# Kernel optimization log

Measured on AMD Instinct MI355X. Metric: run time of the kernel, lower is better.

The kernel has to match this reference:

```python
import jax, jax.numpy as jnp
import numpy as np

B, C, H, W = 8, 256, 64, 64
NH = 4
HD = C // NH
EPS_LN = 1e-5
EPS_NORM = 1e-12


def ln2d(x, w, b):
    # LayerNorm over channel dim of NCHW, per spatial location
    m = jnp.mean(x, axis=1, keepdims=True)
    v = jnp.mean((x - m) ** 2, axis=1, keepdims=True)
    return (x - m) / jnp.sqrt(v + EPS_LN) * w[None, :, None, None] + b[None, :, None, None]


def l2norm(x):
    # F.normalize(x, dim=-1)
    n = jnp.sqrt(jnp.sum(x * x, axis=-1, keepdims=True))
    return x / jnp.maximum(n, EPS_NORM)


def setup_inputs() -> dict:
    key = jax.random.key(0)
    ks = jax.random.split(key, 12)
    s = 0.02
    return {
        "img_feat": jax.random.normal(ks[0], (B, C, H, W), jnp.float32),
        "aux0": jax.random.normal(ks[1], (B, C, H, W), jnp.float32),
        "aux1": jax.random.normal(ks[2], (B, C, H, W), jnp.float32),
        "q_ln_w": jnp.ones((C,), jnp.float32),
        "q_ln_b": jnp.zeros((C,), jnp.float32),
        "kv_ln_w": jnp.ones((C,), jnp.float32),
        "kv_ln_b": jnp.zeros((C,), jnp.float32),
        "Wq": jax.random.normal(ks[3], (C, C), jnp.float32) * s,
        "Wkv": jax.random.normal(ks[4], (2 * C, C), jnp.float32) * s,
        "Wo": jax.random.normal(ks[5], (C, C), jnp.float32) * s,
        "bo": jnp.zeros((C,), jnp.float32),
        "attn_scale": jnp.zeros((NH, 1, 1), jnp.float32),
        "mlp_ln_w": jnp.ones((C,), jnp.float32),
        "mlp_ln_b": jnp.zeros((C,), jnp.float32),
        "W1": jax.random.normal(ks[6], (C, C), jnp.float32) * s,
        "b1": jnp.zeros((C,), jnp.float32),
        "W2": jax.random.normal(ks[7], (C, C), jnp.float32) * s,
        "b2": jnp.zeros((C,), jnp.float32),
    }


def reference(img_feat, aux0, aux1, q_ln_w, q_ln_b, kv_ln_w, kv_ln_b,
              Wq, Wkv, Wo, bo, attn_scale, mlp_ln_w, mlp_ln_b, W1, b1, W2, b2):
    HWn = H * W
    # q branch
    q = ln2d(img_feat, q_ln_w, q_ln_b).reshape(B, C, HWn)
    q = jnp.einsum('oc,bcn->bon', Wq, q).reshape(B, NH, HD, HWn)
    # kv branch: cat aux feats along batch (2B)
    kv_in = jnp.concatenate([aux0, aux1], axis=0)
    kv = ln2d(kv_in, kv_ln_w, kv_ln_b).reshape(2 * B, C, HWn)
    kv = jnp.einsum('oc,bcn->bon', Wkv, kv).reshape(2 * B, 2, NH, HD, HWn)
    k, v = kv[:, 0], kv[:, 1]  # each (2B, nh, hd, hw)
    qn = l2norm(q)
    kn = l2norm(k)
    kt, kd = kn[:B], kn[B:]
    vt, vd = v[:B], v[B:]
    # transposed (cross-covariance) cosine attention: hd x hd score matrix
    tex_attn = jax.nn.softmax(jnp.einsum('bnch,bndh->bncd', qn, kt), axis=-1)
    dep_attn = jax.nn.softmax(jnp.einsum('bnch,bndh->bncd', qn, kd), axis=-1)
    tex_qkv = jnp.einsum('bncd,bndh->bnch', tex_attn, vt)
    dep_qkv = jnp.einsum('bncd,bndh->bnch', dep_attn, vd)
    gate = jax.nn.sigmoid(attn_scale)[None]  # (1, nh, 1, 1)
    qkv = gate * tex_qkv + (1.0 - gate) * dep_qkv  # (B, nh, hd, hw)
    qkv = qkv.reshape(B, C, HWn)
    o = jnp.einsum('oc,bcn->bon', Wo, qkv).reshape(B, C, H, W) + bo[None, :, None, None]
    x = img_feat + o
    # ConvMlp (norm_ffn): LayerNorm2d -> 1x1 conv -> GELU -> 1x1 conv
    y = ln2d(x, mlp_ln_w, mlp_ln_b).reshape(B, C, HWn)
    y = jnp.einsum('oc,bcn->bon', W1, y) + b1[None, :, None]
    y = jax.nn.gelu(y)
    y = jnp.einsum('oc,bcn->bon', W2, y) + b2[None, :, None]
    return x + y.reshape(B, C, H, W)
```

## Files before the change

kernel.cpp:

```cpp
#include <hip/hip_runtime.h>
#include <math.h>
#include <stdint.h>

#define B_   8
#define C_   256
#define N_   4096

typedef __bf16 bf16;
typedef __bf16 bf16x8 __attribute__((ext_vector_type(8)));
typedef __bf16 bf16x4 __attribute__((ext_vector_type(4)));
typedef float  f32x4  __attribute__((ext_vector_type(4)));

#define MFMA16(a, b, c) __builtin_amdgcn_mfma_f32_16x16x32_bf16((a), (b), (c), 0, 0, 0)

struct Ptrs { const void* p[18]; };

__device__ __forceinline__ f32x4 ld4(const void* p, long i, bool f32) {
    f32x4 r;
    if (f32) {
        r = *(const f32x4*)((const float*)p + i);
    } else {
        bf16x4 v = *(const bf16x4*)((const bf16*)p + i);
        r[0] = (float)v[0]; r[1] = (float)v[1]; r[2] = (float)v[2]; r[3] = (float)v[3];
    }
    return r;
}

__device__ __forceinline__ float wave_sum(float s) {
    #pragma unroll
    for (int off = 32; off; off >>= 1) s += __shfl_xor(s, off);
    return s;
}

__device__ __forceinline__ void gl_lds16(const bf16* g, bf16* l) {
    __builtin_amdgcn_global_load_lds(
        (const __attribute__((address_space(1))) void*)(uintptr_t)g,
        (__attribute__((address_space(3))) void*)(uintptr_t)l, 16, 0, 0);
}

__global__ __launch_bounds__(256) void prep_kernel(Ptrs a, bf16* __restrict__ wb,
                                                   float* __restrict__ Sbuf,
                                                   bf16* __restrict__ biasb) {
    bool f32 = ((const unsigned*)a.p[3])[0] == 0x3F800000u;
    int row = blockIdx.x * 4 + (threadIdx.x >> 6);
    int lane = threadIdx.x & 63;
    long c4 = lane * 4;
    if (row >= 1536) {
        if (row == 1539) {
            if (lane == 0) {
                f32x4 v = ld4(a.p[11], 0, f32);
                #pragma unroll
                for (int j = 0; j < 4; ++j) biasb[768 + j] = (bf16)v[j];
            }
        } else {
            const void* s = (row == 1536) ? a.p[10] : (row == 1537) ? a.p[15] : a.p[17];
            f32x4 v = ld4(s, c4, f32);
            bf16x4 o;
            #pragma unroll
            for (int j = 0; j < 4; ++j) o[j] = (bf16)v[j];
            *(bf16x4*)(biasb + (row - 1536) * 256 + c4) = o;
        }
        return;
    }
    const void *W, *lw = nullptr, *lb = nullptr;
    long wrow; bf16* dst; float *s1 = nullptr, *s2 = nullptr;
    if (row < 256)       { W = a.p[7];  lw = a.p[3];  lb = a.p[4];  wrow = row;        dst = wb + row * 256;                 s1 = Sbuf + row;          s2 = Sbuf + 256 + row; }
    else if (row < 768)  { W = a.p[8];  lw = a.p[5];  lb = a.p[6];  wrow = row - 256;  dst = wb + 65536 + wrow * 256;        s1 = Sbuf + 512 + wrow;   s2 = Sbuf + 1024 + wrow; }
    else if (row < 1024) { W = a.p[14]; lw = a.p[12]; lb = a.p[13]; wrow = row - 768;  dst = wb + 196608 + wrow * 256;       s1 = Sbuf + 1536 + wrow;  s2 = Sbuf + 1792 + wrow; }
    else if (row < 1280) { W = a.p[9];  wrow = row - 1024; dst = wb + 262144 + wrow * 256; }
    else                 { W = a.p[16]; wrow = row - 1280; dst = wb + 327680 + wrow * 256; }
    f32x4 W4 = ld4(W, wrow * 256 + c4, f32);
    f32x4 w4, b4;
    if (lw) { w4 = ld4(lw, c4, f32); b4 = ld4(lb, c4, f32); }
    else    { w4[0]=w4[1]=w4[2]=w4[3]=1.f; b4[0]=b4[1]=b4[2]=b4[3]=0.f; }
    bf16x4 o;
    float s1v = 0.f, s2v = 0.f;
    #pragma unroll
    for (int j = 0; j < 4; ++j) {
        float wp = W4[j] * w4[j];
        o[j] = (bf16)wp;
        s1v += wp;
        s2v += W4[j] * b4[j];
    }
    *(bf16x4*)(dst + c4) = o;
    if (s1) {
        s1v = wave_sum(s1v); s2v = wave_sum(s2v);
        if (lane == 0) { *s1 = s1v; *s2 = s2v; }
    }
}

__global__ __launch_bounds__(256) void transpose_kernel(Ptrs a, bf16* __restrict__ xT,
                                                        float2* __restrict__ st) {
    bool f32 = ((const unsigned*)a.p[3])[0] == 0x3F800000u;
    int gt = blockIdx.z;
    const void* src; int batch;
    if (gt < 8)       { src = a.p[0]; batch = gt; }
    else if (gt < 16) { src = a.p[1]; batch = gt - 8; }
    else              { src = a.p[2]; batch = gt - 16; }
    int n0 = blockIdx.x * 64;
    int t = threadIdx.x;
    __shared__ float T[64][68];
    int cl = t >> 4, n4 = (t & 15) * 4;
    int chunk = t & 7, nr = t >> 3;
    float sa[2] = {0.f, 0.f}, qa[2] = {0.f, 0.f};
    for (int ct = 0; ct < 4; ++ct) {
        int c0 = ct * 64;
        if (ct) __syncthreads();
        #pragma unroll
        for (int i = 0; i < 4; ++i) {
            int c = i * 16 + cl;
            f32x4 v = ld4(src, ((long)batch * 256 + c0 + c) * 4096 + n0 + n4, f32);
            #pragma unroll
            for (int j = 0; j < 4; ++j) {
                int nn = n4 + j;
                T[nn][c ^ (((nn >> 2) & 3) << 3)] = v[j];
            }
        }
        __syncthreads();
        #pragma unroll
        for (int j = 0; j < 2; ++j) {
            int n = j * 32 + nr;
            int cs = (chunk * 8) ^ (((n >> 2) & 3) << 3);
            const f32x4* p = (const f32x4*)&T[n][cs];
            f32x4 lo = p[0], hi = p[1];
            bf16x8 o;
            #pragma unroll
            for (int jj = 0; jj < 4; ++jj) { o[jj] = (bf16)lo[jj]; o[4 + jj] = (bf16)hi[jj]; }
            *(bf16x8*)(xT + ((size_t)gt * 4096 + n0 + n) * 256 + c0 + chunk * 8) = o;
            #pragma unroll
            for (int jj = 0; jj < 8; ++jj) { float f = (float)o[jj]; sa[j] += f; qa[j] += f * f; }
        }
    }
    #pragma unroll
    for (int j = 0; j < 2; ++j) {
        float s = sa[j], q = qa[j];
        #pragma unroll
        for (int off = 1; off < 8; off <<= 1) { s += __shfl_xor(s, off); q += __shfl_xor(q, off); }
        if (chunk == 0) {
            float mean = s * (1.0f / 256.0f);
            float var  = q * (1.0f / 256.0f) - mean * mean;
            float2 o2; o2.x = mean; o2.y = rsqrtf(var + 1e-5f);
            st[(size_t)gt * 4096 + n0 + j * 32 + nr] = o2;
        }
    }
}

__global__ __launch_bounds__(256) void statsT_kernel(const bf16* __restrict__ xT,
                                                     float2* __restrict__ st) {
    int row = blockIdx.x * 4 + (threadIdx.x >> 6);
    int lane = threadIdx.x & 63;
    bf16x4 v = *(const bf16x4*)(xT + (size_t)row * 256 + lane * 4);
    float s = 0.f, q = 0.f;
    #pragma unroll
    for (int j = 0; j < 4; ++j) { float f = (float)v[j]; s += f; q += f * f; }
    s = wave_sum(s); q = wave_sum(q);
    if (lane == 0) {
        float mean = s * (1.0f / 256.0f);
        float var  = q * (1.0f / 256.0f) - mean * mean;
        float2 o; o.x = mean; o.y = rsqrtf(var + 1e-5f);
        st[row] = o;
    }
}

__global__ __launch_bounds__(256, 2) void wgemm_kernel(const bf16* __restrict__ A,
                                                    const bf16* __restrict__ xT,
                                                    const float2* __restrict__ stats,
                                                    const float* __restrict__ S1,
                                                    const float* __restrict__ S2,
                                                    const bf16* __restrict__ bias,
                                                    const bf16* __restrict__ resT,
                                                    void* __restrict__ out,
                                                    bf16* __restrict__ vT,
                                                    const unsigned* __restrict__ probe,
                                                    int emode, int gelu) {
    int n0 = blockIdx.x * 128;
    int ot = blockIdx.y;
    int g  = blockIdx.z;
    int t = threadIdx.x, wv = t >> 6, lane = t & 63;
    int m16 = lane & 15, quad = lane >> 4;
    int wr = wv >> 1, wc = wv & 1;
    int rl = lane >> 3, slot = lane & 7;

    __shared__ bf16 As[2][128 * 64];
    __shared__ bf16 Bs[2][128 * 64];

    const bf16* Agbase = A + (size_t)ot * 128 * 256;
    const bf16* Bgbase = xT + ((size_t)g * 4096 + n0) * 256;

    auto stage = [&](int buf, int ks) {
        #pragma unroll
        for (int i = 0; i < 4; ++i) {
            int row = wv * 32 + i * 8 + rl;
            int koff = ks * 64 + ((slot ^ (row & 7)) << 3);
            gl_lds16(Agbase + (size_t)row * 256 + koff, &As[buf][(wv * 32 + i * 8) * 64]);
            gl_lds16(Bgbase + (size_t)row * 256 + koff, &Bs[buf][(wv * 32 + i * 8) * 64]);
        }
    };

    f32x4 acc[4][4];
    #pragma unroll
    for (int i = 0; i < 4; ++i)
        #pragma unroll
        for (int j = 0; j < 4; ++j) acc[i][j] = (f32x4){0.f, 0.f, 0.f, 0.f};

    auto compute = [&](int buf) {
        #pragma unroll
        for (int kf = 0; kf < 2; ++kf) {
            bf16x8 af[4], bv[4];
            #pragma unroll
            for (int mt = 0; mt < 4; ++mt) {
                int r = wr * 64 + mt * 16 + m16;
                af[mt] = *(const bf16x8*)&As[buf][r * 64 + (((kf * 4 + quad) ^ (r & 7)) << 3)];
            }
            #pragma unroll
            for (int nt = 0; nt < 4; ++nt) {
                int r = wc * 64 + nt * 16 + m16;
                bv[nt] = *(const bf16x8*)&Bs[buf][r * 64 + (((kf * 4 + quad) ^ (r & 7)) << 3)];
            }
            #pragma unroll
            for (int mt = 0; mt < 4; ++mt)
                #pragma unroll
                for (int nt = 0; nt < 4; ++nt)
                    acc[mt][nt] = MFMA16(af[mt], bv[nt], acc[mt][nt]);
        }
    };

    stage(0, 0);
    stage(1, 1);
    #pragma unroll
    for (int ks = 0; ks < 4; ++ks) {
        if (ks < 3) asm volatile("s_waitcnt vmcnt(8)" ::: "memory");
        else        asm volatile("s_waitcnt vmcnt(0)" ::: "memory");
        __builtin_amdgcn_sched_barrier(0);
        __builtin_amdgcn_s_barrier();
        compute(ks & 1);
        __builtin_amdgcn_s_barrier();
        if (ks < 2) stage(ks & 1, ks + 2);
    }

    int of32 = (emode == 3) ? (probe[0] == 0x3F800000u) : 0;

    #pragma unroll
    for (int mt = 0; mt < 4; ++mt) {
        int olb  = wr * 64 + mt * 16 + quad * 4;
        int orow = ot * 128 + olb;
        f32x4 s1v, s2v, bz;
        if (stats) { s1v = *(const f32x4*)(S1 + orow); s2v = *(const f32x4*)(S2 + orow); }
        if (bias) {
            bf16x4 bb = *(const bf16x4*)(bias + orow);
            #pragma unroll
            for (int r = 0; r < 4; ++r) bz[r] = (float)bb[r];
        }
        #pragma unroll
        for (int nt = 0; nt < 4; ++nt) {
            int n = n0 + wc * 64 + nt * 16 + m16;
            f32x4 v = acc[mt][nt];
            if (stats) {
                float2 st = stats[(size_t)g * N_ + n];
                float a1 = st.y, a2 = -st.y * st.x;
                #pragma unroll
                for (int r = 0; r < 4; ++r) v[r] = a1 * v[r] + a2 * s1v[r] + s2v[r];
            }
            if (bias) {
                #pragma unroll
                for (int r = 0; r < 4; ++r) v[r] += bz[r];
            }
            if (gelu) {
                #pragma unroll
                for (int r = 0; r < 4; ++r) {
                    float x = v[r];
                    float u = x + 0.044715f * x * x * x;
                    v[r] = 0.5f * x * (1.0f + tanhf(0.7978845608028654f * u));
                }
            }
            if (emode == 0) {
                if (vT == nullptr || orow < 256) {
                    bf16* o = (bf16*)out;
                    #pragma unroll
                    for (int r = 0; r < 4; ++r)
                        o[((size_t)(g * 256 + orow + r)) * N_ + n] = (bf16)v[r];
                } else {
                    int od = orow - 256;
                    int hh = od >> 6, d0 = od & 63;
                    bf16x4 tmp;
                    #pragma unroll
                    for (int r = 0; r < 4; ++r) tmp[r] = (bf16)v[r];
                    *(bf16x4*)(vT + (((size_t)(g * 4 + hh)) * N_ + n) * 64 + d0) = tmp;
                }
            } else if (emode == 2) {
                size_t idx = ((size_t)g * N_ + n) * 256 + orow;
                if (resT) {
                    bf16x4 rr = *(const bf16x4*)(resT + idx);
                    #pragma unroll
                    for (int r = 0; r < 4; ++r) v[r] += (float)rr[r];
                }
                bf16x4 tmp;
                #pragma unroll
                for (int r = 0; r < 4; ++r) tmp[r] = (bf16)v[r];
                *(bf16x4*)((bf16*)out + idx) = tmp;
            } else {
                bf16x4 rr = *(const bf16x4*)(resT + ((size_t)g * N_ + n) * 256 + orow);
                #pragma unroll
                for (int r = 0; r < 4; ++r) {
                    float val = v[r] + (float)rr[r];
                    size_t oi = ((size_t)(g * 256 + orow + r)) * N_ + n;
                    if (of32) ((float*)out)[oi] = val;
                    else      ((bf16*)out)[oi] = (bf16)val;
                }
            }
        }
    }
}

__global__ __launch_bounds__(256) void rownorm_kernel(const bf16* __restrict__ x,
                                                      float* __restrict__ invn) {
    size_t row = blockIdx.x;
    const bf16* p = x + (row << 12);
    int t = threadIdx.x;
    float s = 0.f;
    #pragma unroll
    for (int i = 0; i < 2; ++i) {
        bf16x8 v = *(const bf16x8*)(p + ((size_t)(i * 256 + t) << 3));
        #pragma unroll
        for (int j = 0; j < 8; ++j) { float f = (float)v[j]; s += f * f; }
    }
    #pragma unroll
    for (int off = 32; off > 0; off >>= 1) s += __shfl_down(s, off);
    __shared__ float ps[4];
    if ((t & 63) == 0) ps[t >> 6] = s;
    __syncthreads();
    if (t == 0) {
        float tot = ps[0] + ps[1] + ps[2] + ps[3];
        invn[row] = 1.0f / fmaxf(sqrtf(tot), 1e-12f);
    }
}

__global__ __launch_bounds__(256) void sgemm_kernel(const bf16* __restrict__ q,
                                                    const bf16* __restrict__ k,
                                                    float* __restrict__ Spart) {
    int bh = blockIdx.x, ks = blockIdx.y;
    int b = bh >> 2, h = bh & 3;
    int t = threadIdx.x, wv = t >> 6, lane = t & 63;
    int m16 = lane & 15, quad = lane >> 4;
    const bf16* qrow = q + (size_t)(b * 256 + h * 64 + wv * 16 + m16) * N_;
    const bf16* kt0  = k + (size_t)(b * 256 + h * 64) * N_;
    const bf16* kd0  = k + (size_t)((b + 8) * 256 + h * 64) * N_;

    f32x4 at[4], ad[4];
    #pragma unroll
    for (int i = 0; i < 4; ++i) { at[i] = (f32x4){0.f,0.f,0.f,0.f}; ad[i] = (f32x4){0.f,0.f,0.f,0.f}; }

    int nbeg = ks * 512;
    for (int n = nbeg; n < nbeg + 512; n += 32) {
        int ko = n + quad * 8;
        bf16x8 a = *(const bf16x8*)(qrow + ko);
        #pragma unroll
        for (int dt = 0; dt < 4; ++dt) {
            bf16x8 bt = *(const bf16x8*)(kt0 + (size_t)(dt * 16 + m16) * N_ + ko);
            at[dt] = MFMA16(a, bt, at[dt]);
            bf16x8 bd = *(const bf16x8*)(kd0 + (size_t)(dt * 16 + m16) * N_ + ko);
            ad[dt] = MFMA16(a, bd, ad[dt]);
        }
    }
    float* oT = Spart + (size_t)(ks * 32 + bh) * 4096;
    float* oD = Spart + (size_t)8 * 32 * 4096 + (size_t)(ks * 32 + bh) * 4096;
    #pragma unroll
    for (int dt = 0; dt < 4; ++dt)
        #pragma unroll
        for (int r = 0; r < 4; ++r) {
            int c = wv * 16 + quad * 4 + r, d = dt * 16 + m16;
            oT[c * 64 + d] = at[dt][r];
            oD[c * 64 + d] = ad[dt][r];
        }
}

__global__ __launch_bounds__(256) void softmax_kernel(const float* __restrict__ Spart,
                                                      const float* __restrict__ invnq,
                                                      const float* __restrict__ invnk,
                                                      const bf16* __restrict__ attn_scale,
                                                      bf16* __restrict__ Acat) {
    int bh = blockIdx.x;
    int h = bh & 3;
    int t = threadIdx.x, wv = t >> 6, lane = t & 63;
    float g = 1.0f / (1.0f + expf(-(float)attn_scale[h]));
    #pragma unroll
    for (int i = 0; i < 4; ++i) {
        int idx = blockIdx.y * 16 + wv * 4 + i;
        int stream = idx >> 6, c = idx & 63;
        const float* Sp = Spart + (size_t)stream * 8 * 32 * 4096 + (size_t)bh * 4096 + c * 64 + lane;
        float s = 0.f;
        #pragma unroll
        for (int ks = 0; ks < 8; ++ks) s += Sp[(size_t)ks * 32 * 4096];
        s *= invnq[bh * 64 + c] * invnk[(stream ? bh + 32 : bh) * 64 + lane];
        float mx = s;
        #pragma unroll
        for (int off = 32; off > 0; off >>= 1) mx = fmaxf(mx, __shfl_xor(mx, off));
        float e = expf(s - mx);
        float sum = e;
        #pragma unroll
        for (int off = 32; off > 0; off >>= 1) sum += __shfl_xor(sum, off);
        float a = e / sum * (stream == 0 ? g : 1.0f - g);
        Acat[(size_t)bh * 8192 + c * 128 + stream * 64 + lane] = (bf16)a;
    }
}

__global__ __launch_bounds__(256) void av_kernel(const bf16* __restrict__ Acat,
                                                 const bf16* __restrict__ vT,
                                                 bf16* __restrict__ qkvT) {
    int pt = blockIdx.x, h = blockIdx.y, b = blockIdx.z;
    int bh = b * 4 + h;
    int t = threadIdx.x, wv = t >> 6, lane = t & 63;
    int m16 = lane & 15, quad = lane >> 4;
    int p0 = pt * 64;

    const bf16* Arow = Acat + (size_t)bh * 8192 + (size_t)(wv * 16 + m16) * 128 + quad * 8;
    bf16x8 a[4];
    #pragma unroll
    for (int ds = 0; ds < 4; ++ds) a[ds] = *(const bf16x8*)(Arow + ds * 32);

    f32x4 acc[4];
    #pragma unroll
    for (int i = 0; i < 4; ++i) acc[i] = (f32x4){0.f,0.f,0.f,0.f};

    #pragma unroll
    for (int nt = 0; nt < 4; ++nt) {
        int p = p0 + nt * 16 + m16;
        #pragma unroll
        for (int ds = 0; ds < 4; ++ds) {
            int stream = ds >> 1;
            int dl = (ds & 1) * 32 + quad * 8;
            const bf16* vb = vT + (((size_t)(b + 8 * stream) * 4 + h) * N_ + p) * 64 + dl;
            bf16x8 bv = *(const bf16x8*)vb;
            acc[nt] = MFMA16(a[ds], bv, acc[nt]);
        }
    }
    #pragma unroll
    for (int nt = 0; nt < 4; ++nt) {
        int p = p0 + nt * 16 + m16;
        int cbase = h * 64 + wv * 16 + quad * 4;
        bf16x4 o;
        #pragma unroll
        for (int r = 0; r < 4; ++r) o[r] = (bf16)acc[nt][r];
        *(bf16x4*)(qkvT + ((size_t)b * 4096 + p) * 256 + cbase) = o;
    }
}

extern "C" void kernel_launch(void* const* d_in, const int* in_sizes, int n_in,
                              void* d_out, int out_size, void* d_ws, size_t ws_size,
                              hipStream_t stream) {
    (void)in_sizes; (void)n_in; (void)out_size; (void)ws_size;

    Ptrs args;
    for (int i = 0; i < 18; ++i) args.p[i] = d_in[i];
    const unsigned* probe = (const unsigned*)d_in[3];

    char* ws = (char*)d_ws;
    size_t off = 0;
    auto alloc = [&](size_t bytes) { char* p = ws + off; off += (bytes + 255) & ~(size_t)255; return p; };
    bf16*   xTall = (bf16*)alloc(50331648);
    float2* stAll = (float2*)alloc(786432);
    float2* stX   = (float2*)alloc(262144);
    bf16*   wb    = (bf16*)alloc(786432);
    float*  Sbuf  = (float*)alloc(8192);
    bf16*   biasb = (bf16*)alloc(2048);
    bf16*   q     = (bf16*)alloc(16777216);
    bf16*   k     = (bf16*)alloc(33554432);
    bf16*   vT    = (bf16*)alloc(33554432);
    float*  Spart = (float*)alloc(8388608);
    bf16*   Acat  = (bf16*)alloc(524288);
    float*  invnq = (float*)alloc(8192);
    float*  invnk = (float*)alloc(16384);

    bf16* imgT  = xTall;
    bf16* auxT  = xTall + (size_t)8 * 4096 * 256;
    bf16* qkvT  = q;
    bf16* xbufT = k;
    bf16* h1T   = auxT;

    prep_kernel<<<385, 256, 0, stream>>>(args, wb, Sbuf, biasb);
    transpose_kernel<<<dim3(64, 1, 24), 256, 0, stream>>>(args, xTall, stAll);
    wgemm_kernel<<<dim3(32, 2, 8),  256, 0, stream>>>(wb,         imgT, stAll,            Sbuf,       Sbuf + 256,  nullptr, nullptr, q, nullptr, probe, 0, 0);
    wgemm_kernel<<<dim3(32, 4, 16), 256, 0, stream>>>(wb + 65536, auxT, stAll + 8 * 4096, Sbuf + 512, Sbuf + 1024, nullptr, nullptr, k, vT,      probe, 0, 0);
    rownorm_kernel<<<2048, 256, 0, stream>>>(q, invnq);
    rownorm_kernel<<<4096, 256, 0, stream>>>(k, invnk);
    sgemm_kernel<<<dim3(32, 8), 256, 0, stream>>>(q, k, Spart);
    softmax_kernel<<<dim3(32, 8), 256, 0, stream>>>(Spart, invnq, invnk, biasb + 768, Acat);
    av_kernel<<<dim3(64, 4, 8), 256, 0, stream>>>(Acat, vT, qkvT);
    wgemm_kernel<<<dim3(32, 2, 8), 256, 0, stream>>>(wb + 262144, qkvT, nullptr, nullptr, nullptr, biasb, imgT, xbufT, nullptr, probe, 2, 0);
    statsT_kernel<<<8192, 256, 0, stream>>>(xbufT, stX);
    wgemm_kernel<<<dim3(32, 2, 8), 256, 0, stream>>>(wb + 196608, xbufT, stX, Sbuf + 1536, Sbuf + 1792, biasb + 256, nullptr, h1T, nullptr, probe, 2, 1);
    wgemm_kernel<<<dim3(32, 2, 8), 256, 0, stream>>>(wb + 327680, h1T, nullptr, nullptr, nullptr, biasb + 512, xbufT, d_out, nullptr, probe, 3, 0);
}
```

Baseline: 382.1 us.

## Stage GEMM and AV epilogues through LDS for coalesced 16-byte stores

```diff
diff --git a/kernel.cpp b/kernel.cpp
--- a/kernel.cpp
+++ b/kernel.cpp
@@ -181,8 +181,10 @@
     int wr = wv >> 1, wc = wv & 1;
     int rl = lane >> 3, slot = lane & 7;
 
-    __shared__ bf16 As[2][128 * 64];
-    __shared__ bf16 Bs[2][128 * 64];
+    __shared__ char smem[65536];
+    bf16* As = (bf16*)smem;
+    bf16* Bs = (bf16*)(smem + 32768);
+    bf16* E  = (bf16*)smem;
 
     const bf16* Agbase = A + (size_t)ot * 128 * 256;
     const bf16* Bgbase = xT + ((size_t)g * 4096 + n0) * 256;
@@ -192,8 +194,8 @@
         for (int i = 0; i < 4; ++i) {
             int row = wv * 32 + i * 8 + rl;
             int koff = ks * 64 + ((slot ^ (row & 7)) << 3);
-            gl_lds16(Agbase + (size_t)row * 256 + koff, &As[buf][(wv * 32 + i * 8) * 64]);
-            gl_lds16(Bgbase + (size_t)row * 256 + koff, &Bs[buf][(wv * 32 + i * 8) * 64]);
+            gl_lds16(Agbase + (size_t)row * 256 + koff, &As[buf * 8192 + (wv * 32 + i * 8) * 64]);
+            gl_lds16(Bgbase + (size_t)row * 256 + koff, &Bs[buf * 8192 + (wv * 32 + i * 8) * 64]);
         }
     };
 
@@ -210,12 +212,12 @@
             #pragma unroll
             for (int mt = 0; mt < 4; ++mt) {
                 int r = wr * 64 + mt * 16 + m16;
-                af[mt] = *(const bf16x8*)&As[buf][r * 64 + (((kf * 4 + quad) ^ (r & 7)) << 3)];
+                af[mt] = *(const bf16x8*)&As[buf * 8192 + r * 64 + (((kf * 4 + quad) ^ (r & 7)) << 3)];
             }
             #pragma unroll
             for (int nt = 0; nt < 4; ++nt) {
                 int r = wc * 64 + nt * 16 + m16;
-                bv[nt] = *(const bf16x8*)&Bs[buf][r * 64 + (((kf * 4 + quad) ^ (r & 7)) << 3)];
+                bv[nt] = *(const bf16x8*)&Bs[buf * 8192 + r * 64 + (((kf * 4 + quad) ^ (r & 7)) << 3)];
             }
             #pragma unroll
             for (int mt = 0; mt < 4; ++mt)
@@ -238,7 +240,34 @@
         if (ks < 2) stage(ks & 1, ks + 2);
     }
 
-    int of32 = (emode == 3) ? (probe[0] == 0x3F800000u) : 0;
+    bool natural = (emode == 0) && (vT == nullptr || ot < 2);
+
+    if (emode == 3) {
+        int of32 = (probe[0] == 0x3F800000u);
+        #pragma unroll
+        for (int mt = 0; mt < 4; ++mt) {
+            int olb  = wr * 64 + mt * 16 + quad * 4;
+            int orow = ot * 128 + olb;
+            f32x4 bz;
+            bf16x4 bb = *(const bf16x4*)(bias + orow);
+            #pragma unroll
+            for (int r = 0; r < 4; ++r) bz[r] = (float)bb[r];
+            #pragma unroll
+            for (int nt = 0; nt < 4; ++nt) {
+                int n = n0 + wc * 64 + nt * 16 + m16;
+                f32x4 v = acc[mt][nt];
+                bf16x4 rr = *(const bf16x4*)(resT + ((size_t)g * N_ + n) * 256 + orow);
+                #pragma unroll
+                for (int r = 0; r < 4; ++r) {
+                    float val = v[r] + bz[r] + (float)rr[r];
+                    size_t oi = ((size_t)(g * 256 + orow + r)) * N_ + n;
+                    if (of32) ((float*)out)[oi] = val;
+                    else      ((bf16*)out)[oi] = (bf16)val;
+                }
+            }
+        }
+        return;
+    }
 
     #pragma unroll
     for (int mt = 0; mt < 4; ++mt) {
@@ -253,7 +282,8 @@
         }
         #pragma unroll
         for (int nt = 0; nt < 4; ++nt) {
-            int n = n0 + wc * 64 + nt * 16 + m16;
+            int nloc = wc * 64 + nt * 16 + m16;
+            int n = n0 + nloc;
             f32x4 v = acc[mt][nt];
             if (stats) {
                 float2 st = stats[(size_t)g * N_ + n];
@@ -273,41 +303,51 @@
                     v[r] = 0.5f * x * (1.0f + tanhf(0.7978845608028654f * u));
                 }
             }
-            if (emode == 0) {
-                if (vT == nullptr || orow < 256) {
-                    bf16* o = (bf16*)out;
-                    #pragma unroll
-                    for (int r = 0; r < 4; ++r)
-                        o[((size_t)(g * 256 + orow + r)) * N_ + n] = (bf16)v[r];
-                } else {
-                    int od = orow - 256;
-                    int hh = od >> 6, d0 = od & 63;
-                    bf16x4 tmp;
-                    #pragma unroll
-                    for (int r = 0; r < 4; ++r) tmp[r] = (bf16)v[r];
-                    *(bf16x4*)(vT + (((size_t)(g * 4 + hh)) * N_ + n) * 64 + d0) = tmp;
-                }
-            } else if (emode == 2) {
-                size_t idx = ((size_t)g * N_ + n) * 256 + orow;
-                if (resT) {
-                    bf16x4 rr = *(const bf16x4*)(resT + idx);
-                    #pragma unroll
-                    for (int r = 0; r < 4; ++r) v[r] += (float)rr[r];
-                }
+            if (natural) {
+                #pragma unroll
+                for (int r = 0; r < 4; ++r) E[(olb + r) * 136 + nloc] = (bf16)v[r];
+            } else {
                 bf16x4 tmp;
                 #pragma unroll
                 for (int r = 0; r < 4; ++r) tmp[r] = (bf16)v[r];
-                *(bf16x4*)((bf16*)out + idx) = tmp;
-            } else {
-                bf16x4 rr = *(const bf16x4*)(resT + ((size_t)g * N_ + n) * 256 + orow);
-                #pragma unroll
-                for (int r = 0; r < 4; ++r) {
-                    float val = v[r] + (float)rr[r];
-                    size_t oi = ((size_t)(g * 256 + orow + r)) * N_ + n;
-                    if (of32) ((float*)out)[oi] = val;
-                    else      ((bf16*)out)[oi] = (bf16)val;
-                }
-            }
+                *(bf16x4*)&E[nloc * 136 + olb] = tmp;
+            }
+        }
+    }
+    __syncthreads();
+
+    if (natural) {
+        bf16* o = (bf16*)out;
+        #pragma unroll
+        for (int i = 0; i < 8; ++i) {
+            int idx = i * 256 + t;
+            int ro = idx >> 4, co = idx & 15;
+            bf16x8 v = *(const bf16x8*)&E[ro * 136 + co * 8];
+            *(bf16x8*)(o + (size_t)(g * 256 + ot * 128 + ro) * N_ + n0 + co * 8) = v;
+        }
+    } else if (emode == 0) {
+        #pragma unroll
+        for (int i = 0; i < 8; ++i) {
+            int idx = i * 256 + t;
+            int nr = idx >> 4, ch = idx & 15;
+            int hh2 = ch >> 3, c8 = (ch & 7) * 8;
+            bf16x8 v = *(const bf16x8*)&E[nr * 136 + hh2 * 64 + c8];
+            int hh = (ot - 2) * 2 + hh2;
+            *(bf16x8*)(vT + (((size_t)(g * 4 + hh)) * N_ + n0 + nr) * 64 + c8) = v;
+        }
+    } else {
+        #pragma unroll
+        for (int i = 0; i < 8; ++i) {
+            int idx = i * 256 + t;
+            int nr = idx >> 4, ch = idx & 15;
+            bf16x8 v = *(const bf16x8*)&E[nr * 136 + ch * 8];
+            size_t gi = ((size_t)g * N_ + n0 + nr) * 256 + ot * 128 + ch * 8;
+            if (resT) {
+                bf16x8 rr = *(const bf16x8*)(resT + gi);
+                #pragma unroll
+                for (int j = 0; j < 8; ++j) v[j] = (bf16)((float)v[j] + (float)rr[j]);
+            }
+            *(bf16x8*)((bf16*)out + gi) = v;
         }
     }
 }
@@ -412,6 +452,7 @@
     int t = threadIdx.x, wv = t >> 6, lane = t & 63;
     int m16 = lane & 15, quad = lane >> 4;
     int p0 = pt * 64;
+    __shared__ bf16 E2[64 * 72];
 
     const bf16* Arow = Acat + (size_t)bh * 8192 + (size_t)(wv * 16 + m16) * 128 + quad * 8;
     bf16x8 a[4];
@@ -436,12 +477,20 @@
     }
     #pragma unroll
     for (int nt = 0; nt < 4; ++nt) {
-        int p = p0 + nt * 16 + m16;
-        int cbase = h * 64 + wv * 16 + quad * 4;
+        int pl = nt * 16 + m16;
+        int cl = wv * 16 + quad * 4;
         bf16x4 o;
         #pragma unroll
         for (int r = 0; r < 4; ++r) o[r] = (bf16)acc[nt][r];
-        *(bf16x4*)(qkvT + ((size_t)b * 4096 + p) * 256 + cbase) = o;
+        *(bf16x4*)&E2[pl * 72 + cl] = o;
+    }
+    __syncthreads();
+    #pragma unroll
+    for (int i = 0; i < 2; ++i) {
+        int idx = i * 256 + t;
+        int pr = idx >> 3, ch = idx & 7;
+        bf16x8 v = *(const bf16x8*)&E2[pr * 72 + ch * 8];
+        *(bf16x8*)(qkvT + ((size_t)b * 4096 + p0 + pr) * 256 + h * 64 + ch * 8) = v;
     }
 }
 
```

Result: faster. 360.4 us (-5.7%).
